# Kernel optimization log

Measured on AMD Instinct MI355X. Metric: run time of the kernel, lower is better.

Reference implementation:

```python
import jax, jax.numpy as jnp
import numpy as np

B, N, D, H = 2, 512, 32, 64

def custom_norm(x):
    # forward of tf custom_norm (stabilization only affects the gradient)
    return jnp.linalg.norm(x, axis=-1, keepdims=True)

def vecvec(a, b):
    """vector*vector -> (scalar, e12, e13, e23); identical math to the swizzle tensordot."""
    s = jnp.sum(a * b, axis=-1, keepdims=True)
    e12 = a[..., 0:1] * b[..., 1:2] - a[..., 1:2] * b[..., 0:1]
    e13 = a[..., 0:1] * b[..., 2:3] - a[..., 2:3] * b[..., 0:1]
    e23 = a[..., 1:2] * b[..., 2:3] - a[..., 2:3] * b[..., 1:2]
    return jnp.concatenate([s, e12, e13, e23], axis=-1)

def setup_inputs() -> dict:
    key = jax.random.key(0)
    ks = jax.random.split(key, 8)
    return {
        "positions": jax.random.normal(ks[0], (B, N, 3), jnp.float32),
        "values": jax.random.normal(ks[1], (B, N, D), jnp.float32),
        "W1": jax.random.normal(ks[2], (2, H), jnp.float32) * (2.0 / 2.0) ** 0.5,
        "b1": jnp.zeros((H,), jnp.float32),
        "W2": jax.random.normal(ks[3], (H, D), jnp.float32) * (2.0 / H) ** 0.5,
        "b2": jnp.zeros((D,), jnp.float32),
        "Ws1": jax.random.normal(ks[4], (D, H), jnp.float32) * (2.0 / D) ** 0.5,
        "bs1": jnp.zeros((H,), jnp.float32),
        "Ws2": jax.random.normal(ks[5], (H, 1), jnp.float32) * (2.0 / H) ** 0.5,
        "bs2": jnp.zeros((1,), jnp.float32),
    }

def reference(positions, values, W1, b1, W2, b2, Ws1, bs1, Ws2, bs2):
    # rank-2 tuple expansion (broadcast_indices): left varies last particle axis,
    # right varies second-to-last particle axis.
    r_left = positions[..., None, :, :]    # (B,1,N,3)
    r_right = positions[..., :, None, :]   # (B,N,1,3)
    prod = vecvec(r_left, r_right)         # (B,N,N,4) scalar + bivector
    # vecvec_invariants: scalar and bivector norm -> (B,N,N,2)
    invar = jnp.concatenate([prod[..., :1], custom_norm(prod[..., 1:4])], axis=-1)
    # merge_fun='mean' over the two tuple positions of the per-particle values
    neigh = 0.5 * (values[..., None, :, :] + values[..., :, None, :])  # (B,N,N,D)
    # value_net: Dense(H, relu) -> Dense(D)
    invar_values = jax.nn.relu(invar @ W1 + b1) @ W2 + b2              # (B,N,N,D)
    # join_fun='mean'
    joined = 0.5 * (invar_values + neigh)                              # (B,N,N,D)
    # score_net: Dense(H, relu) -> Dense(1)
    scores = jax.nn.relu(joined @ Ws1 + bs1) @ Ws2 + bs2               # (B,N,N,1)
    # reduce=True: softmax over all N*N*1 tuple scores per batch element
    attention = jax.nn.softmax(scores.reshape(scores.shape[0], -1), axis=-1)
    attention = attention.reshape(scores.shape)
    # weighted sum over both tuple axes (tuple_weights == 1, no weights input)
    return jnp.sum(attention * joined, axis=(-3, -2))                  # (B,D)
```

## Files before the change

kernel.cpp:

```cpp
#include <hip/hip_runtime.h>
#include <math.h>

#define BB 2
#define NN 512
#define DD 32
#define HH 64
#define JT 2
#define NBLK1 (BB*NN*JT)

#define MF_OFF  0
#define WF_OFF  (MF_OFF + 2048)
#define W1F_OFF (WF_OFF + 1024)
#define ST2_OFF (W1F_OFF + 128)
#define AR_OFF  (ST2_OFF + 4096)

typedef _Float16 half8 __attribute__((ext_vector_type(8)));
typedef float    f32x4 __attribute__((ext_vector_type(4)));

__device__ __forceinline__ half8 h8splat(float v) {
    _Float16 h = (_Float16)v;
    half8 r = {h,h,h,h,h,h,h,h};
    return r;
}

__device__ __forceinline__ void invar2(float pix, float piy, float piz,
                                       float pjx, float pjy, float pjz,
                                       float& s, float& cr) {
    s = pix*pjx + piy*pjy + piz*pjz;
    float e12 = pjx*piy - pjy*pix;
    float e13 = pjx*piz - pjz*pix;
    float e23 = pjy*piz - pjz*piy;
    cr = sqrtf(e12*e12 + e13*e13 + e23*e23);
}

#define R2 4096
#define R3 2048
#define R4 192
#define PREP_T (R2+R3+R4)

__global__ __launch_bounds__(256) void prep(const float* __restrict__ W1,
                                            const float* __restrict__ b1,
                                            const float* __restrict__ W2,
                                            const float* __restrict__ Ws1,
                                            float* __restrict__ ws) {
    int idx = blockIdx.x * 256 + threadIdx.x;
    if (idx < R2) {
        int e = idx;
        int t = e & 7, lane = (e >> 3) & 63, f = e >> 9;
        int cf = f >> 1, kh = f & 1;
        int k   = kh*32 + 8*(lane >> 4) + t;
        int col = cf*16 + (lane & 15);
        float acc = 0.f;
        #pragma unroll
        for (int d = 0; d < DD; d++) acc += W2[k*DD + d] * Ws1[d*HH + col];
        ((_Float16*)(ws + MF_OFF))[e] = (_Float16)(0.5f * acc);
    } else if (idx < R2+R3) {
        int e = idx - R2;
        int t = e & 7, lane = (e >> 3) & 63, cf = e >> 9;
        int k   = 8*(lane >> 4) + t;
        int col = cf*16 + (lane & 15);
        ((_Float16*)(ws + WF_OFF))[e] = (_Float16)(0.25f * Ws1[k*HH + col]);
    } else if (idx < R2+R3+R4) {
        int e = idx - R2 - R3;
        int t = e & 7, rest = e >> 3;
        int g = rest & 3, kh = (rest >> 2) & 1, arr = rest >> 3;
        int k = kh*32 + 8*g + t;
        float v = (arr == 0) ? W1[k] : (arr == 1) ? W1[HH + k] : b1[k];
        ((_Float16*)(ws + W1F_OFF))[e] = (_Float16)v;
    }
}

__global__ __launch_bounds__(256) void pass1(const float* __restrict__ pos,
                                             const float* __restrict__ values,
                                             const float* __restrict__ b2,
                                             const float* __restrict__ Ws1,
                                             const float* __restrict__ bs1,
                                             const float* __restrict__ Ws2,
                                             const float* __restrict__ bs2,
                                             float* __restrict__ ws) {
    __shared__ float uqc[HH];
    __shared__ float ws2l[HH];
    __shared__ float lA[4][HH];
    __shared__ float lms[4][2];
    int blk = blockIdx.x;
    int jt = blk & 1;
    int i  = (blk >> 1) & (NN-1);
    int b  = blk >> 10;
    int tid = threadIdx.x;
    int w    = tid >> 6;
    int lane = tid & 63;
    int g    = lane >> 4;
    int lr   = lane & 15;

    if (tid < HH) {
        const float* vrow = values + (size_t)(b*NN + i)*DD;
        float acc = bs1[tid];
        #pragma unroll
        for (int d = 0; d < DD; d++) acc += (0.25f*vrow[d] + 0.5f*b2[d]) * Ws1[d*HH + tid];
        uqc[tid]  = acc;
        ws2l[tid] = Ws2[tid];
    }

    const half8* mf8 = (const half8*)(ws + MF_OFF);
    const half8* wf8 = (const half8*)(ws + WF_OFF);
    half8 Bf[4][2], Wf[4];
    #pragma unroll
    for (int cf = 0; cf < 4; cf++) {
        Bf[cf][0] = mf8[(cf*2 + 0)*64 + lane];
        Bf[cf][1] = mf8[(cf*2 + 1)*64 + lane];
        Wf[cf]    = wf8[cf*64 + lane];
    }
    const half8* w1f8 = (const half8*)(ws + W1F_OFF);
    half8 W1a[2], W1b[2], B1f[2];
    #pragma unroll
    for (int kh = 0; kh < 2; kh++) {
        W1a[kh] = w1f8[(0*2 + kh)*4 + g];
        W1b[kh] = w1f8[(1*2 + kh)*4 + g];
        B1f[kh] = w1f8[(2*2 + kh)*4 + g];
    }

    float pix = pos[(b*NN+i)*3+0], piy = pos[(b*NN+i)*3+1], piz = pos[(b*NN+i)*3+2];
    float bs2v = bs2[0];
    half8 z8 = h8splat(0.f);

    __syncthreads();

    float m_run = -INFINITY, s_run = 0.f;
    float Ak[16];
    #pragma unroll
    for (int t = 0; t < 16; t++) Ak[t] = 0.f;

    #pragma unroll
    for (int rf = 0; rf < 4; rf++) {
        int j_a = jt*256 + w*64 + rf*16 + lr;
        float pjx = pos[(b*NN+j_a)*3+0], pjy = pos[(b*NN+j_a)*3+1], pjz = pos[(b*NN+j_a)*3+2];
        const float* vj = values + (size_t)(b*NN + j_a)*DD + 8*g;
        half8 A2;
        #pragma unroll
        for (int t = 0; t < 8; t++) A2[t] = (_Float16)vj[t];

        float s, cr;
        invar2(pix,piy,piz,pjx,pjy,pjz,s,cr);
        half8 s8 = h8splat(s), c8 = h8splat(cr);
        half8 A0 = __builtin_elementwise_max(W1a[0]*s8 + W1b[0]*c8 + B1f[0], z8);
        half8 A1 = __builtin_elementwise_max(W1a[1]*s8 + W1b[1]*c8 + B1f[1], z8);

        f32x4 c[4];
        #pragma unroll
        for (int cf = 0; cf < 4; cf++) {
            f32x4 z = {0.f, 0.f, 0.f, 0.f};
            z = __builtin_amdgcn_mfma_f32_16x16x32_f16(A0, Bf[cf][0], z, 0, 0, 0);
            z = __builtin_amdgcn_mfma_f32_16x16x32_f16(A1, Bf[cf][1], z, 0, 0, 0);
            c[cf] = __builtin_amdgcn_mfma_f32_16x16x32_f16(A2, Wf[cf], z, 0, 0, 0);
        }

        float part0 = 0.f, part1 = 0.f, part2 = 0.f, part3 = 0.f;
        #pragma unroll
        for (int cf = 0; cf < 4; cf++) {
            int lc = cf*16 + lr;
            float base = uqc[lc];
            float w2v  = ws2l[lc];
            part0 += fmaxf(c[cf][0] + base, 0.f) * w2v;
            part1 += fmaxf(c[cf][1] + base, 0.f) * w2v;
            part2 += fmaxf(c[cf][2] + base, 0.f) * w2v;
            part3 += fmaxf(c[cf][3] + base, 0.f) * w2v;
        }
        #pragma unroll
        for (int m = 1; m < 16; m <<= 1) {
            part0 += __shfl_xor(part0, m);
            part1 += __shfl_xor(part1, m);
            part2 += __shfl_xor(part2, m);
            part3 += __shfl_xor(part3, m);
        }
        float x0 = part0 + bs2v, x1 = part1 + bs2v, x2 = part2 + bs2v, x3 = part3 + bs2v;

        int src = (lr >> 2) << 4;
        float y0 = __shfl(x0, src);
        float y1 = __shfl(x1, src);
        float y2 = __shfl(x2, src);
        float y3 = __shfl(x3, src);
        float t01 = (lr & 1) ? y1 : y0;
        float t23 = (lr & 1) ? y3 : y2;
        float x_own = (lr & 2) ? t23 : t01;

        float mm = fmaxf(fmaxf(x0, x1), fmaxf(x2, x3));
        float nm = fmaxf(m_run, mm);
        float rsc = __expf(m_run - nm);
        s_run = s_run*rsc
              + __expf(x0 - nm) + __expf(x1 - nm) + __expf(x2 - nm) + __expf(x3 - nm);
        float w_own = __expf(x_own - nm);
        #pragma unroll
        for (int t = 0; t < 8; t++) Ak[t]   = fmaf(Ak[t],   rsc, w_own * (float)A0[t]);
        #pragma unroll
        for (int t = 0; t < 8; t++) Ak[8+t] = fmaf(Ak[8+t], rsc, w_own * (float)A1[t]);
        m_run = nm;
    }

    float mg = m_run;
    #pragma unroll
    for (int off = 16; off < 64; off <<= 1) {
        float om = __shfl_xor(m_run, off);
        float os = __shfl_xor(s_run, off);
        float nm = fmaxf(m_run, om);
        s_run = s_run*__expf(m_run - nm) + os*__expf(om - nm);
        m_run = nm;
    }
    #pragma unroll
    for (int t = 0; t < 16; t++) {
        #pragma unroll
        for (int msk = 1; msk < 16; msk <<= 1) Ak[t] += __shfl_xor(Ak[t], msk);
    }
    float gsc = __expf(mg - m_run);
    if (lr == 0) {
        #pragma unroll
        for (int t = 0; t < 8; t++) lA[w][8*g + t]      = Ak[t]   * gsc;
        #pragma unroll
        for (int t = 0; t < 8; t++) lA[w][32 + 8*g + t] = Ak[8+t] * gsc;
    }
    if (lane == 0) { lms[w][0] = m_run; lms[w][1] = s_run; }
    __syncthreads();

    if (tid < HH) {
        float m0 = lms[0][0], m1 = lms[1][0], m2 = lms[2][0], m3 = lms[3][0];
        float mB = fmaxf(fmaxf(m0, m1), fmaxf(m2, m3));
        float e0 = __expf(m0 - mB), e1 = __expf(m1 - mB);
        float e2 = __expf(m2 - mB), e3 = __expf(m3 - mB);
        float ar = lA[0][tid]*e0 + lA[1][tid]*e1 + lA[2][tid]*e2 + lA[3][tid]*e3;
        ws[AR_OFF + (size_t)blk*HH + tid] = ar;
        if (tid == 0) {
            float sB = lms[0][1]*e0 + lms[1][1]*e1 + lms[2][1]*e2 + lms[3][1]*e3;
            ws[ST2_OFF + blk*2]     = mB;
            ws[ST2_OFF + blk*2 + 1] = sB;
        }
    }
}

__global__ __launch_bounds__(256) void finalk(const float* __restrict__ values,
                                              const float* __restrict__ W2,
                                              const float* __restrict__ b2,
                                              const float* __restrict__ ws,
                                              float* __restrict__ out) {
    __shared__ float red[8];
    __shared__ float MS[2];
    __shared__ float wf[NN*JT];
    __shared__ float csh[NN];
    __shared__ float vs8[8][DD];
    __shared__ float as4[4][HH];
    __shared__ float Ash[HH];
    int b = blockIdx.x;
    int tid = threadIdx.x;
    int w = tid >> 6, lane = tid & 63;
    const float* st2 = ws + ST2_OFF + (size_t)b*NN*JT*2;

    {
        float m = -INFINITY, s = 0.f;
        #pragma unroll
        for (int q = 0; q < 4; q++) {
            int p = tid + q*256;
            float pm = st2[p*2], ps = st2[p*2+1];
            float nm = fmaxf(m, pm);
            s = s*__expf(m - nm) + ps*__expf(pm - nm);
            m = nm;
        }
        for (int off = 1; off < 64; off <<= 1) {
            float om = __shfl_xor(m, off);
            float os = __shfl_xor(s, off);
            float nm = fmaxf(m, om);
            s = s*__expf(m - nm) + os*__expf(om - nm);
            m = nm;
        }
        if (lane == 0) { red[w*2] = m; red[w*2+1] = s; }
    }
    __syncthreads();
    if (tid == 0) {
        float M0 = red[0], S0 = red[1];
        #pragma unroll
        for (int q = 1; q < 4; q++) {
            float nm = fmaxf(M0, red[q*2]);
            S0 = S0*__expf(M0 - nm) + red[q*2+1]*__expf(red[q*2] - nm);
            M0 = nm;
        }
        MS[0] = M0; MS[1] = 1.f / S0;
    }
    __syncthreads();
    float M = MS[0], invS = MS[1];

    #pragma unroll
    for (int q = 0; q < 4; q++) {
        int p = tid + q*256;
        wf[p] = __expf(st2[p*2] - M) * invS;
    }
    __syncthreads();
    #pragma unroll
    for (int q = 0; q < 2; q++) {
        int i = tid + q*256;
        csh[i] = st2[(2*i)*2+1]*wf[2*i] + st2[(2*i+1)*2+1]*wf[2*i+1];
    }
    __syncthreads();

    {
        int d = tid & 31, sl = tid >> 5;
        float v = 0.f;
        for (int i = sl*64; i < sl*64 + 64; i++)
            v += csh[i] * values[(size_t)(b*NN + i)*DD + d];
        vs8[sl][d] = v;
    }
    {
        int k = tid & 63, sl = tid >> 6;
        const float* ar = ws + AR_OFF + (size_t)b*NN*JT*HH;
        float a = 0.f;
        for (int p = sl*256; p < sl*256 + 256; p++)
            a += ar[(size_t)p*HH + k] * wf[p];
        as4[sl][k] = a;
    }
    __syncthreads();
    if (tid < HH) Ash[tid] = as4[0][tid] + as4[1][tid] + as4[2][tid] + as4[3][tid];
    __syncthreads();
    if (tid < DD) {
        float vsum = 0.f;
        #pragma unroll
        for (int q = 0; q < 8; q++) vsum += vs8[q][tid];
        float aw = 0.f;
        #pragma unroll
        for (int k = 0; k < HH; k++) aw += Ash[k] * W2[k*DD + tid];
        out[b*DD + tid] = 0.5f*b2[tid] + 0.5f*aw + 0.5f*vsum;
    }
}

extern "C" void kernel_launch(void* const* d_in, const int* in_sizes, int n_in,
                              void* d_out, int out_size, void* d_ws, size_t ws_size,
                              hipStream_t stream) {
    (void)in_sizes; (void)n_in; (void)out_size; (void)ws_size;
    const float* pos    = (const float*)d_in[0];
    const float* values = (const float*)d_in[1];
    const float* W1     = (const float*)d_in[2];
    const float* b1     = (const float*)d_in[3];
    const float* W2     = (const float*)d_in[4];
    const float* b2     = (const float*)d_in[5];
    const float* Ws1    = (const float*)d_in[6];
    const float* bs1    = (const float*)d_in[7];
    const float* Ws2    = (const float*)d_in[8];
    const float* bs2    = (const float*)d_in[9];
    float* ws  = (float*)d_ws;
    float* out = (float*)d_out;

    prep  <<<(PREP_T + 255)/256, 256, 0, stream>>>(W1, b1, W2, Ws1, ws);
    pass1 <<<NBLK1, 256, 0, stream>>>(pos, values, b2, Ws1, bs1, Ws2, bs2, ws);
    finalk<<<BB, 256, 0, stream>>>(values, W2, b2, ws, out);
}
```

Before: 45.54 us.

## Precompute per-row score bias in prep and restructure attention-weighted hidden accumulation

Moves the per-(b,i) uqc computation (a 32-long dot product per hidden unit) out of pass1 into the prep kernel, writing it to workspace so each pass1 block only loads it. The online rescaled per-lane accumulation of hidden activations with 16-register shuffle reductions is replaced by a different scheme. Scores and invariants are stashed in shared memory, exponentiated against the block max after the reduction, and a per-hidden-unit loop recomputes the ReLU hidden value in fp32 and accumulates the weighted sum. Value loads become float4 vector loads. This adds extra shared-memory traffic and block barriers, plus a larger prep kernel.

```diff
diff --git a/kernel.cpp b/kernel.cpp
--- a/kernel.cpp
+++ b/kernel.cpp
@@ -11,7 +11,8 @@
 #define MF_OFF  0
 #define WF_OFF  (MF_OFF + 2048)
 #define W1F_OFF (WF_OFF + 1024)
-#define ST2_OFF (W1F_OFF + 128)
+#define UQC_OFF (W1F_OFF + 128)
+#define ST2_OFF (UQC_OFF + BB*NN*HH)
 #define AR_OFF  (ST2_OFF + 4096)
 
 typedef _Float16 half8 __attribute__((ext_vector_type(8)));
@@ -36,12 +37,16 @@
 #define R2 4096
 #define R3 2048
 #define R4 192
-#define PREP_T (R2+R3+R4)
-
-__global__ __launch_bounds__(256) void prep(const float* __restrict__ W1,
+#define R5 (BB*NN*HH)
+#define PREP_T (R2+R3+R4+R5)
+
+__global__ __launch_bounds__(256) void prep(const float* __restrict__ values,
+                                            const float* __restrict__ W1,
                                             const float* __restrict__ b1,
                                             const float* __restrict__ W2,
+                                            const float* __restrict__ b2,
                                             const float* __restrict__ Ws1,
+                                            const float* __restrict__ bs1,
                                             float* __restrict__ ws) {
     int idx = blockIdx.x * 256 + threadIdx.x;
     if (idx < R2) {
@@ -67,21 +72,30 @@
         int k = kh*32 + 8*g + t;
         float v = (arr == 0) ? W1[k] : (arr == 1) ? W1[HH + k] : b1[k];
         ((_Float16*)(ws + W1F_OFF))[e] = (_Float16)v;
+    } else if (idx < PREP_T) {
+        int e = idx - R2 - R3 - R4;
+        int l = e & 63; int n = (e >> 6) & (NN-1); int b = e >> 15;
+        const float* vrow = values + (size_t)(b*NN + n)*DD;
+        float acc = bs1[l];
+        #pragma unroll
+        for (int d = 0; d < DD; d++) acc += (0.25f*vrow[d] + 0.5f*b2[d]) * Ws1[d*HH + l];
+        ws[UQC_OFF + e] = acc;
     }
 }
 
 __global__ __launch_bounds__(256) void pass1(const float* __restrict__ pos,
                                              const float* __restrict__ values,
-                                             const float* __restrict__ b2,
-                                             const float* __restrict__ Ws1,
-                                             const float* __restrict__ bs1,
+                                             const float* __restrict__ W1,
+                                             const float* __restrict__ b1,
                                              const float* __restrict__ Ws2,
                                              const float* __restrict__ bs2,
                                              float* __restrict__ ws) {
     __shared__ float uqc[HH];
     __shared__ float ws2l[HH];
-    __shared__ float lA[4][HH];
+    __shared__ float sc[256];
+    __shared__ float sA[256], cA[256];
     __shared__ float lms[4][2];
+    __shared__ float Aw[4][HH];
     int blk = blockIdx.x;
     int jt = blk & 1;
     int i  = (blk >> 1) & (NN-1);
@@ -93,11 +107,7 @@
     int lr   = lane & 15;
 
     if (tid < HH) {
-        const float* vrow = values + (size_t)(b*NN + i)*DD;
-        float acc = bs1[tid];
-        #pragma unroll
-        for (int d = 0; d < DD; d++) acc += (0.25f*vrow[d] + 0.5f*b2[d]) * Ws1[d*HH + tid];
-        uqc[tid]  = acc;
+        uqc[tid]  = ws[UQC_OFF + ((size_t)(b*NN + i))*HH + tid];
         ws2l[tid] = Ws2[tid];
     }
 
@@ -126,21 +136,22 @@
     __syncthreads();
 
     float m_run = -INFINITY, s_run = 0.f;
-    float Ak[16];
-    #pragma unroll
-    for (int t = 0; t < 16; t++) Ak[t] = 0.f;
 
     #pragma unroll
     for (int rf = 0; rf < 4; rf++) {
-        int j_a = jt*256 + w*64 + rf*16 + lr;
+        int jl  = w*64 + rf*16 + lr;
+        int j_a = jt*256 + jl;
         float pjx = pos[(b*NN+j_a)*3+0], pjy = pos[(b*NN+j_a)*3+1], pjz = pos[(b*NN+j_a)*3+2];
         const float* vj = values + (size_t)(b*NN + j_a)*DD + 8*g;
+        float4 va = *(const float4*)(vj);
+        float4 vb = *(const float4*)(vj + 4);
         half8 A2;
-        #pragma unroll
-        for (int t = 0; t < 8; t++) A2[t] = (_Float16)vj[t];
+        A2[0]=(_Float16)va.x; A2[1]=(_Float16)va.y; A2[2]=(_Float16)va.z; A2[3]=(_Float16)va.w;
+        A2[4]=(_Float16)vb.x; A2[5]=(_Float16)vb.y; A2[6]=(_Float16)vb.z; A2[7]=(_Float16)vb.w;
 
         float s, cr;
         invar2(pix,piy,piz,pjx,pjy,pjz,s,cr);
+        if (g == 0) { sA[jl] = s; cA[jl] = cr; }
         half8 s8 = h8splat(s), c8 = h8splat(cr);
         half8 A0 = __builtin_elementwise_max(W1a[0]*s8 + W1b[0]*c8 + B1f[0], z8);
         half8 A1 = __builtin_elementwise_max(W1a[1]*s8 + W1b[1]*c8 + B1f[1], z8);
@@ -174,29 +185,18 @@
         }
         float x0 = part0 + bs2v, x1 = part1 + bs2v, x2 = part2 + bs2v, x3 = part3 + bs2v;
 
-        int src = (lr >> 2) << 4;
-        float y0 = __shfl(x0, src);
-        float y1 = __shfl(x1, src);
-        float y2 = __shfl(x2, src);
-        float y3 = __shfl(x3, src);
-        float t01 = (lr & 1) ? y1 : y0;
-        float t23 = (lr & 1) ? y3 : y2;
-        float x_own = (lr & 2) ? t23 : t01;
+        float xs01 = (lr & 1) ? x1 : x0;
+        float xs23 = (lr & 1) ? x3 : x2;
+        float xsel = (lr & 2) ? xs23 : xs01;
+        if (lr < 4) sc[w*64 + rf*16 + 4*g + lr] = xsel;
 
         float mm = fmaxf(fmaxf(x0, x1), fmaxf(x2, x3));
         float nm = fmaxf(m_run, mm);
-        float rsc = __expf(m_run - nm);
-        s_run = s_run*rsc
+        s_run = s_run*__expf(m_run - nm)
               + __expf(x0 - nm) + __expf(x1 - nm) + __expf(x2 - nm) + __expf(x3 - nm);
-        float w_own = __expf(x_own - nm);
-        #pragma unroll
-        for (int t = 0; t < 8; t++) Ak[t]   = fmaf(Ak[t],   rsc, w_own * (float)A0[t]);
-        #pragma unroll
-        for (int t = 0; t < 8; t++) Ak[8+t] = fmaf(Ak[8+t], rsc, w_own * (float)A1[t]);
         m_run = nm;
     }
 
-    float mg = m_run;
     #pragma unroll
     for (int off = 16; off < 64; off <<= 1) {
         float om = __shfl_xor(m_run, off);
@@ -205,33 +205,33 @@
         s_run = s_run*__expf(m_run - nm) + os*__expf(om - nm);
         m_run = nm;
     }
-    #pragma unroll
-    for (int t = 0; t < 16; t++) {
-        #pragma unroll
-        for (int msk = 1; msk < 16; msk <<= 1) Ak[t] += __shfl_xor(Ak[t], msk);
-    }
-    float gsc = __expf(mg - m_run);
-    if (lr == 0) {
-        #pragma unroll
-        for (int t = 0; t < 8; t++) lA[w][8*g + t]      = Ak[t]   * gsc;
-        #pragma unroll
-        for (int t = 0; t < 8; t++) lA[w][32 + 8*g + t] = Ak[8+t] * gsc;
-    }
     if (lane == 0) { lms[w][0] = m_run; lms[w][1] = s_run; }
     __syncthreads();
 
-    if (tid < HH) {
-        float m0 = lms[0][0], m1 = lms[1][0], m2 = lms[2][0], m3 = lms[3][0];
-        float mB = fmaxf(fmaxf(m0, m1), fmaxf(m2, m3));
-        float e0 = __expf(m0 - mB), e1 = __expf(m1 - mB);
-        float e2 = __expf(m2 - mB), e3 = __expf(m3 - mB);
-        float ar = lA[0][tid]*e0 + lA[1][tid]*e1 + lA[2][tid]*e2 + lA[3][tid]*e3;
-        ws[AR_OFF + (size_t)blk*HH + tid] = ar;
-        if (tid == 0) {
-            float sB = lms[0][1]*e0 + lms[1][1]*e1 + lms[2][1]*e2 + lms[3][1]*e3;
-            ws[ST2_OFF + blk*2]     = mB;
-            ws[ST2_OFF + blk*2 + 1] = sB;
-        }
+    float m0 = lms[0][0], m1 = lms[1][0], m2 = lms[2][0], m3 = lms[3][0];
+    float mB = fmaxf(fmaxf(m0, m1), fmaxf(m2, m3));
+    float sB = lms[0][1]*__expf(m0 - mB) + lms[1][1]*__expf(m1 - mB)
+             + lms[2][1]*__expf(m2 - mB) + lms[3][1]*__expf(m3 - mB);
+    sc[tid] = __expf(sc[tid] - mB);
+    __syncthreads();
+
+    float w1a = W1[lane], w1b = W1[HH + lane], b1l = b1[lane];
+    float Ak = 0.f;
+    int p0 = w * 64;
+    #pragma unroll 4
+    for (int p = p0; p < p0 + 64; p++) {
+        float s = sA[p], cr = cA[p], wgt = sc[p];
+        float h = fmaxf(fmaf(w1a, s, fmaf(w1b, cr, b1l)), 0.f);
+        Ak = fmaf(wgt, h, Ak);
+    }
+    Aw[w][lane] = Ak;
+    __syncthreads();
+
+    if (tid < HH)
+        ws[AR_OFF + (size_t)blk*HH + tid] = Aw[0][tid] + Aw[1][tid] + Aw[2][tid] + Aw[3][tid];
+    if (tid == 0) {
+        ws[ST2_OFF + blk*2]     = mB;
+        ws[ST2_OFF + blk*2 + 1] = sB;
     }
 }
 
@@ -344,7 +344,7 @@
     float* ws  = (float*)d_ws;
     float* out = (float*)d_out;
 
-    prep  <<<(PREP_T + 255)/256, 256, 0, stream>>>(W1, b1, W2, Ws1, ws);
-    pass1 <<<NBLK1, 256, 0, stream>>>(pos, values, b2, Ws1, bs1, Ws2, bs2, ws);
+    prep  <<<(PREP_T + 255)/256, 256, 0, stream>>>(values, W1, b1, W2, b2, Ws1, bs1, ws);
+    pass1 <<<NBLK1, 256, 0, stream>>>(pos, values, W1, b1, Ws2, bs2, ws);
     finalk<<<BB, 256, 0, stream>>>(values, W2, b2, ws, out);
 }
```

Measured after the change: 44.28 us. 1.03x faster.

## Transpose MFMA operands in pass1 to drop per-block uqc precompute and shuffles

Applied to the files above, without the earlier changes.

Swaps the MFMA operand roles so the weight fragments are the A operand and the per-j hidden activations are the B operand. The per-row values term and b2 are folded into the B vector (v_j + v_i + 2*b2), and bs1 is folded into the accumulator init. This removes the per-block 64x32 uqc precompute, its shared-memory reads and the first __syncthreads. The 16-lane shuffle reductions and x_own broadcast are replaced by two xor-shuffles. Online softmax rescaling of the H accumulators is replaced by a two-phase scheme: block max first, then a weighted accumulation. The change also adds __launch_bounds__(256,2) and keeps bh fragments live across the loop, which adds register pressure.

```diff
diff --git a/kernel.cpp b/kernel.cpp
--- a/kernel.cpp
+++ b/kernel.cpp
@@ -47,19 +47,19 @@
     if (idx < R2) {
         int e = idx;
         int t = e & 7, lane = (e >> 3) & 63, f = e >> 9;
-        int cf = f >> 1, kh = f & 1;
-        int k   = kh*32 + 8*(lane >> 4) + t;
-        int col = cf*16 + (lane & 15);
+        int lt = f >> 1, kh = f & 1;
+        int k = kh*32 + 8*(lane >> 4) + t;
+        int l = lt*16 + (lane & 15);
         float acc = 0.f;
         #pragma unroll
-        for (int d = 0; d < DD; d++) acc += W2[k*DD + d] * Ws1[d*HH + col];
+        for (int d = 0; d < DD; d++) acc += W2[k*DD + d] * Ws1[d*HH + l];
         ((_Float16*)(ws + MF_OFF))[e] = (_Float16)(0.5f * acc);
     } else if (idx < R2+R3) {
         int e = idx - R2;
-        int t = e & 7, lane = (e >> 3) & 63, cf = e >> 9;
-        int k   = 8*(lane >> 4) + t;
-        int col = cf*16 + (lane & 15);
-        ((_Float16*)(ws + WF_OFF))[e] = (_Float16)(0.25f * Ws1[k*HH + col]);
+        int t = e & 7, lane = (e >> 3) & 63, lt = e >> 9;
+        int d = 8*(lane >> 4) + t;
+        int l = lt*16 + (lane & 15);
+        ((_Float16*)(ws + WF_OFF))[e] = (_Float16)(0.25f * Ws1[d*HH + l]);
     } else if (idx < R2+R3+R4) {
         int e = idx - R2 - R3;
         int t = e & 7, rest = e >> 3;
@@ -70,18 +70,15 @@
     }
 }
 
-__global__ __launch_bounds__(256) void pass1(const float* __restrict__ pos,
-                                             const float* __restrict__ values,
-                                             const float* __restrict__ b2,
-                                             const float* __restrict__ Ws1,
-                                             const float* __restrict__ bs1,
-                                             const float* __restrict__ Ws2,
-                                             const float* __restrict__ bs2,
-                                             float* __restrict__ ws) {
-    __shared__ float uqc[HH];
-    __shared__ float ws2l[HH];
-    __shared__ float lA[4][HH];
+__global__ __launch_bounds__(256, 2) void pass1(const float* __restrict__ pos,
+                                                const float* __restrict__ values,
+                                                const float* __restrict__ b2,
+                                                const float* __restrict__ bs1,
+                                                const float* __restrict__ Ws2,
+                                                const float* __restrict__ bs2,
+                                                float* __restrict__ ws) {
     __shared__ float lms[4][2];
+    __shared__ float Aw[4][HH];
     int blk = blockIdx.x;
     int jt = blk & 1;
     int i  = (blk >> 1) & (NN-1);
@@ -92,23 +89,14 @@
     int g    = lane >> 4;
     int lr   = lane & 15;
 
-    if (tid < HH) {
-        const float* vrow = values + (size_t)(b*NN + i)*DD;
-        float acc = bs1[tid];
-        #pragma unroll
-        for (int d = 0; d < DD; d++) acc += (0.25f*vrow[d] + 0.5f*b2[d]) * Ws1[d*HH + tid];
-        uqc[tid]  = acc;
-        ws2l[tid] = Ws2[tid];
-    }
-
     const half8* mf8 = (const half8*)(ws + MF_OFF);
     const half8* wf8 = (const half8*)(ws + WF_OFF);
-    half8 Bf[4][2], Wf[4];
-    #pragma unroll
-    for (int cf = 0; cf < 4; cf++) {
-        Bf[cf][0] = mf8[(cf*2 + 0)*64 + lane];
-        Bf[cf][1] = mf8[(cf*2 + 1)*64 + lane];
-        Wf[cf]    = wf8[cf*64 + lane];
+    half8 AfM[4][2], AfW[4];
+    #pragma unroll
+    for (int lt = 0; lt < 4; lt++) {
+        AfM[lt][0] = mf8[(lt*2 + 0)*64 + lane];
+        AfM[lt][1] = mf8[(lt*2 + 1)*64 + lane];
+        AfW[lt]    = wf8[lt*64 + lane];
     }
     const half8* w1f8 = (const half8*)(ws + W1F_OFF);
     half8 W1a[2], W1b[2], B1f[2];
@@ -119,120 +107,123 @@
         B1f[kh] = w1f8[(2*2 + kh)*4 + g];
     }
 
+    float ws2g[16], bs1g[16];
+    #pragma unroll
+    for (int lt = 0; lt < 4; lt++)
+        #pragma unroll
+        for (int r = 0; r < 4; r++) {
+            int l = lt*16 + 4*g + r;
+            ws2g[lt*4+r] = Ws2[l];
+            bs1g[lt*4+r] = bs1[l];
+        }
+
+    float vip[8];
+    {
+        const float* vi = values + (size_t)(b*NN + i)*DD + 8*g;
+        float4 a = *(const float4*)vi;
+        float4 c = *(const float4*)(vi + 4);
+        const float* b2s = b2 + 8*g;
+        float4 ba = *(const float4*)b2s;
+        float4 bc = *(const float4*)(b2s + 4);
+        vip[0]=a.x+2.f*ba.x; vip[1]=a.y+2.f*ba.y; vip[2]=a.z+2.f*ba.z; vip[3]=a.w+2.f*ba.w;
+        vip[4]=c.x+2.f*bc.x; vip[5]=c.y+2.f*bc.y; vip[6]=c.z+2.f*bc.z; vip[7]=c.w+2.f*bc.w;
+    }
+
     float pix = pos[(b*NN+i)*3+0], piy = pos[(b*NN+i)*3+1], piz = pos[(b*NN+i)*3+2];
     float bs2v = bs2[0];
     half8 z8 = h8splat(0.f);
 
-    __syncthreads();
-
-    float m_run = -INFINITY, s_run = 0.f;
-    float Ak[16];
-    #pragma unroll
-    for (int t = 0; t < 16; t++) Ak[t] = 0.f;
+    half8 bh0[4], bh1[4];
+    float x[4];
+    float m_l = -INFINITY, s_l = 0.f;
 
     #pragma unroll
     for (int rf = 0; rf < 4; rf++) {
-        int j_a = jt*256 + w*64 + rf*16 + lr;
-        float pjx = pos[(b*NN+j_a)*3+0], pjy = pos[(b*NN+j_a)*3+1], pjz = pos[(b*NN+j_a)*3+2];
-        const float* vj = values + (size_t)(b*NN + j_a)*DD + 8*g;
-        half8 A2;
-        #pragma unroll
-        for (int t = 0; t < 8; t++) A2[t] = (_Float16)vj[t];
-
+        int j = jt*256 + w*64 + rf*16 + lr;
+        float pjx = pos[(b*NN+j)*3+0], pjy = pos[(b*NN+j)*3+1], pjz = pos[(b*NN+j)*3+2];
         float s, cr;
         invar2(pix,piy,piz,pjx,pjy,pjz,s,cr);
         half8 s8 = h8splat(s), c8 = h8splat(cr);
-        half8 A0 = __builtin_elementwise_max(W1a[0]*s8 + W1b[0]*c8 + B1f[0], z8);
-        half8 A1 = __builtin_elementwise_max(W1a[1]*s8 + W1b[1]*c8 + B1f[1], z8);
-
-        f32x4 c[4];
-        #pragma unroll
-        for (int cf = 0; cf < 4; cf++) {
-            f32x4 z = {0.f, 0.f, 0.f, 0.f};
-            z = __builtin_amdgcn_mfma_f32_16x16x32_f16(A0, Bf[cf][0], z, 0, 0, 0);
-            z = __builtin_amdgcn_mfma_f32_16x16x32_f16(A1, Bf[cf][1], z, 0, 0, 0);
-            c[cf] = __builtin_amdgcn_mfma_f32_16x16x32_f16(A2, Wf[cf], z, 0, 0, 0);
-        }
-
-        float part0 = 0.f, part1 = 0.f, part2 = 0.f, part3 = 0.f;
-        #pragma unroll
-        for (int cf = 0; cf < 4; cf++) {
-            int lc = cf*16 + lr;
-            float base = uqc[lc];
-            float w2v  = ws2l[lc];
-            part0 += fmaxf(c[cf][0] + base, 0.f) * w2v;
-            part1 += fmaxf(c[cf][1] + base, 0.f) * w2v;
-            part2 += fmaxf(c[cf][2] + base, 0.f) * w2v;
-            part3 += fmaxf(c[cf][3] + base, 0.f) * w2v;
-        }
-        #pragma unroll
-        for (int m = 1; m < 16; m <<= 1) {
-            part0 += __shfl_xor(part0, m);
-            part1 += __shfl_xor(part1, m);
-            part2 += __shfl_xor(part2, m);
-            part3 += __shfl_xor(part3, m);
-        }
-        float x0 = part0 + bs2v, x1 = part1 + bs2v, x2 = part2 + bs2v, x3 = part3 + bs2v;
-
-        int src = (lr >> 2) << 4;
-        float y0 = __shfl(x0, src);
-        float y1 = __shfl(x1, src);
-        float y2 = __shfl(x2, src);
-        float y3 = __shfl(x3, src);
-        float t01 = (lr & 1) ? y1 : y0;
-        float t23 = (lr & 1) ? y3 : y2;
-        float x_own = (lr & 2) ? t23 : t01;
-
-        float mm = fmaxf(fmaxf(x0, x1), fmaxf(x2, x3));
-        float nm = fmaxf(m_run, mm);
-        float rsc = __expf(m_run - nm);
-        s_run = s_run*rsc
-              + __expf(x0 - nm) + __expf(x1 - nm) + __expf(x2 - nm) + __expf(x3 - nm);
-        float w_own = __expf(x_own - nm);
-        #pragma unroll
-        for (int t = 0; t < 8; t++) Ak[t]   = fmaf(Ak[t],   rsc, w_own * (float)A0[t]);
-        #pragma unroll
-        for (int t = 0; t < 8; t++) Ak[8+t] = fmaf(Ak[8+t], rsc, w_own * (float)A1[t]);
-        m_run = nm;
-    }
-
-    float mg = m_run;
-    #pragma unroll
-    for (int off = 16; off < 64; off <<= 1) {
-        float om = __shfl_xor(m_run, off);
-        float os = __shfl_xor(s_run, off);
-        float nm = fmaxf(m_run, om);
-        s_run = s_run*__expf(m_run - nm) + os*__expf(om - nm);
-        m_run = nm;
+        bh0[rf] = __builtin_elementwise_max(W1a[0]*s8 + W1b[0]*c8 + B1f[0], z8);
+        bh1[rf] = __builtin_elementwise_max(W1a[1]*s8 + W1b[1]*c8 + B1f[1], z8);
+
+        const float* vj = values + (size_t)(b*NN + j)*DD + 8*g;
+        float4 va = *(const float4*)vj;
+        float4 vb = *(const float4*)(vj + 4);
+        half8 Bv;
+        Bv[0]=(_Float16)(va.x+vip[0]); Bv[1]=(_Float16)(va.y+vip[1]);
+        Bv[2]=(_Float16)(va.z+vip[2]); Bv[3]=(_Float16)(va.w+vip[3]);
+        Bv[4]=(_Float16)(vb.x+vip[4]); Bv[5]=(_Float16)(vb.y+vip[5]);
+        Bv[6]=(_Float16)(vb.z+vip[6]); Bv[7]=(_Float16)(vb.w+vip[7]);
+
+        float xp = 0.f;
+        #pragma unroll
+        for (int lt = 0; lt < 4; lt++) {
+            f32x4 c = {bs1g[lt*4+0], bs1g[lt*4+1], bs1g[lt*4+2], bs1g[lt*4+3]};
+            c = __builtin_amdgcn_mfma_f32_16x16x32_f16(AfM[lt][0], bh0[rf], c, 0, 0, 0);
+            c = __builtin_amdgcn_mfma_f32_16x16x32_f16(AfM[lt][1], bh1[rf], c, 0, 0, 0);
+            c = __builtin_amdgcn_mfma_f32_16x16x32_f16(AfW[lt],    Bv,      c, 0, 0, 0);
+            xp += fmaxf(c[0], 0.f)*ws2g[lt*4+0];
+            xp += fmaxf(c[1], 0.f)*ws2g[lt*4+1];
+            xp += fmaxf(c[2], 0.f)*ws2g[lt*4+2];
+            xp += fmaxf(c[3], 0.f)*ws2g[lt*4+3];
+        }
+        xp += __shfl_xor(xp, 16);
+        xp += __shfl_xor(xp, 32);
+        float xs = xp + bs2v;
+        x[rf] = xs;
+        float nm = fmaxf(m_l, xs);
+        s_l = s_l*__expf(m_l - nm) + __expf(xs - nm);
+        m_l = nm;
+    }
+
+    #pragma unroll
+    for (int off = 1; off < 16; off <<= 1) {
+        float om = __shfl_xor(m_l, off);
+        float os = __shfl_xor(s_l, off);
+        float nm = fmaxf(m_l, om);
+        s_l = s_l*__expf(m_l - nm) + os*__expf(om - nm);
+        m_l = nm;
+    }
+    if (lane == 0) { lms[w][0] = m_l; lms[w][1] = s_l; }
+    __syncthreads();
+
+    float m0 = lms[0][0], m1 = lms[1][0], m2 = lms[2][0], m3 = lms[3][0];
+    float mB = fmaxf(fmaxf(m0, m1), fmaxf(m2, m3));
+    float sB = lms[0][1]*__expf(m0 - mB) + lms[1][1]*__expf(m1 - mB)
+             + lms[2][1]*__expf(m2 - mB) + lms[3][1]*__expf(m3 - mB);
+    if (tid == 0) {
+        ws[ST2_OFF + blk*2]     = mB;
+        ws[ST2_OFF + blk*2 + 1] = sB;
+    }
+
+    float Ak[16];
+    #pragma unroll
+    for (int t = 0; t < 16; t++) Ak[t] = 0.f;
+    #pragma unroll
+    for (int rf = 0; rf < 4; rf++) {
+        float wgt = __expf(x[rf] - mB);
+        #pragma unroll
+        for (int t = 0; t < 8; t++) {
+            Ak[t]   = fmaf(wgt, (float)bh0[rf][t], Ak[t]);
+            Ak[8+t] = fmaf(wgt, (float)bh1[rf][t], Ak[8+t]);
+        }
     }
     #pragma unroll
     for (int t = 0; t < 16; t++) {
         #pragma unroll
-        for (int msk = 1; msk < 16; msk <<= 1) Ak[t] += __shfl_xor(Ak[t], msk);
-    }
-    float gsc = __expf(mg - m_run);
+        for (int off = 1; off < 16; off <<= 1) Ak[t] += __shfl_xor(Ak[t], off);
+    }
     if (lr == 0) {
         #pragma unroll
-        for (int t = 0; t < 8; t++) lA[w][8*g + t]      = Ak[t]   * gsc;
-        #pragma unroll
-        for (int t = 0; t < 8; t++) lA[w][32 + 8*g + t] = Ak[8+t] * gsc;
-    }
-    if (lane == 0) { lms[w][0] = m_run; lms[w][1] = s_run; }
-    __syncthreads();
-
-    if (tid < HH) {
-        float m0 = lms[0][0], m1 = lms[1][0], m2 = lms[2][0], m3 = lms[3][0];
-        float mB = fmaxf(fmaxf(m0, m1), fmaxf(m2, m3));
-        float e0 = __expf(m0 - mB), e1 = __expf(m1 - mB);
-        float e2 = __expf(m2 - mB), e3 = __expf(m3 - mB);
-        float ar = lA[0][tid]*e0 + lA[1][tid]*e1 + lA[2][tid]*e2 + lA[3][tid]*e3;
-        ws[AR_OFF + (size_t)blk*HH + tid] = ar;
-        if (tid == 0) {
-            float sB = lms[0][1]*e0 + lms[1][1]*e1 + lms[2][1]*e2 + lms[3][1]*e3;
-            ws[ST2_OFF + blk*2]     = mB;
-            ws[ST2_OFF + blk*2 + 1] = sB;
-        }
-    }
+        for (int t = 0; t < 8; t++) {
+            Aw[w][8*g + t]      = Ak[t];
+            Aw[w][32 + 8*g + t] = Ak[8+t];
+        }
+    }
+    __syncthreads();
+    if (tid < HH)
+        ws[AR_OFF + (size_t)blk*HH + tid] = Aw[0][tid] + Aw[1][tid] + Aw[2][tid] + Aw[3][tid];
 }
 
 __global__ __launch_bounds__(256) void finalk(const float* __restrict__ values,
@@ -345,6 +336,6 @@
     float* out = (float*)d_out;
 
     prep  <<<(PREP_T + 255)/256, 256, 0, stream>>>(W1, b1, W2, Ws1, ws);
-    pass1 <<<NBLK1, 256, 0, stream>>>(pos, values, b2, Ws1, bs1, Ws2, bs2, ws);
+    pass1 <<<NBLK1, 256, 0, stream>>>(pos, values, b2, bs1, Ws2, bs2, ws);
     finalk<<<BB, 256, 0, stream>>>(values, W2, b2, ws, out);
 }
```

Measured after the change: 42.63 us (median of 2 runs). -6.4%, faster.
